# Performance work log

Hardware: AMD Instinct MI355X
Metric: run time of the kernel (lower is better)

The kernel has to match this reference:

```python
import jax, jax.numpy as jnp
import numpy as np

B, S, H = 1, 2048, 1024
NH, HD = 16, 64
WIN = 512
M_MEM, M_PER = 512, 64
SCALE = 1.0 / np.sqrt(HD)
NEG_INF = jnp.float32(-1e30)


def setup_inputs() -> dict:
    key = jax.random.key(0)
    ks = jax.random.split(key, 22)
    std = 1.0 / np.sqrt(H)
    def w(k):
        return (jax.random.normal(k, (H, H), jnp.float32) * std)
    names = ['local_wq','local_wk','local_wv','local_wo',
             'long_wq','long_wk','long_wv','long_wo',
             'mem_wq','mem_wk','mem_wv','mem_wo',
             'per_wq','per_wk','per_wv','per_wo']
    d = {n: w(ks[i]) for i, n in enumerate(names)}
    d['gate_w'] = jax.random.normal(ks[16], (4 * H, 4), jnp.float32) * 0.02
    d['gate_b'] = jnp.zeros((4,), jnp.float32)
    d['x'] = jax.random.normal(ks[17], (B, S, H), jnp.float32)
    d['memory_kv'] = jax.random.normal(ks[18], (B, M_MEM, H), jnp.float32)
    d['persona_kv'] = jax.random.normal(ks[19], (B, M_PER, H), jnp.float32)
    return d


def _split_heads(t):
    # (B, T, H) -> (B, NH, T, HD)
    b, t_, _ = t.shape
    return t.reshape(b, t_, NH, HD).transpose(0, 2, 1, 3)


def _merge_heads(t):
    b, h, t_, d = t.shape
    return t.transpose(0, 2, 1, 3).reshape(b, t_, h * d)


def _self_attn(x, wq, wk, wv, wo, mask):
    # mask: (S, S) bool, True = masked out
    q = _split_heads(x @ wq)
    k = _split_heads(x @ wk)
    v = _split_heads(x @ wv)
    scores = jnp.einsum('bhsd,bhtd->bhst', q, k) * SCALE
    scores = jnp.where(mask[None, None], NEG_INF, scores)
    a = jax.nn.softmax(scores, axis=-1)
    out = jnp.einsum('bhst,bhtd->bhsd', a, v)
    return _merge_heads(out) @ wo


def _cross_attn(x, ctx, wq, wk, wv, wo):
    q = _split_heads(x @ wq)
    k = _split_heads(ctx @ wk)
    v = _split_heads(ctx @ wv)
    scores = jnp.einsum('bhsd,bhmd->bhsm', q, k) * SCALE
    a = jax.nn.softmax(scores, axis=-1)
    out = jnp.einsum('bhsm,bhmd->bhsd', a, v)
    return _merge_heads(out) @ wo


def reference(x, memory_kv, persona_kv,
              local_wq, local_wk, local_wv, local_wo,
              long_wq, long_wk, long_wv, long_wo,
              mem_wq, mem_wk, mem_wv, mem_wo,
              per_wq, per_wk, per_wv, per_wo,
              gate_w, gate_b):
    s = x.shape[1]
    idx = jnp.arange(s)
    causal = idx[None, :] > idx[:, None]                    # future tokens masked
    local = causal | ((idx[:, None] - idx[None, :]) > WIN)  # sliding window + causal

    local_out = _self_attn(x, local_wq, local_wk, local_wv, local_wo, local)
    long_out = _self_attn(x, long_wq, long_wk, long_wv, long_wo, causal)
    mem_out = _cross_attn(x, memory_kv, mem_wq, mem_wk, mem_wv, mem_wo)
    per_out = _cross_attn(x, persona_kv, per_wq, per_wk, per_wv, per_wo)

    outs = (local_out, long_out, mem_out, per_out)
    gate_in = jnp.concatenate(outs, axis=-1)                # (B, S, 4H)
    gates = jax.nn.softmax(gate_in @ gate_w + gate_b, axis=-1)  # (B, S, 4)
    fused = sum(gates[..., i:i + 1] * o for i, o in enumerate(outs))
    return fused  # emotion_scale = 1.0, dropout off (eval)
```

## Files before the change

### kernel.cpp

```cpp
#include <hip/hip_runtime.h>

#define S 2048
#define H 1024
#define NH 16
#define HD 64
#define WIN 512
#define SCALE_Q 0.18033688f
#define SM_SHIFT 16.0f

typedef unsigned short u16;
typedef unsigned int u32;
typedef __attribute__((ext_vector_type(8))) short bfrag;
typedef __attribute__((ext_vector_type(4))) float facc;
typedef __attribute__((ext_vector_type(4))) unsigned short u16x4;

#define VMCNT(n) asm volatile("s_waitcnt vmcnt(" #n ")" ::: "memory")

constexpr size_t M1    = 1u << 20;
constexpr size_t WTO   = 0;
constexpr size_t XBO   = 8 * M1;
constexpr size_t MEMBO = 10 * M1;
constexpr size_t PERBO = MEMBO + (M1 >> 1);
constexpr size_t QO    = PERBO + (M1 >> 4);
constexpr size_t KVO   = QO + 8 * M1;
constexpr size_t K2O   = KVO + 8 * M1;
constexpr size_t V2O   = K2O + (M1 >> 1);
constexpr size_t K3O   = V2O + (M1 >> 1);
constexpr size_t V3O   = K3O + (M1 >> 4);
constexpr size_t VT1O  = V3O + (M1 >> 4);
constexpr size_t VT2O  = VT1O + 2 * M1;
constexpr size_t VT3O  = VT2O + (M1 >> 1);
constexpr size_t RECSZ = 8704;

__device__ __forceinline__ u16 f2bf(float f) {
    union { float f; unsigned u; } v; v.f = f;
    unsigned r = v.u + 0x7fffu + ((v.u >> 16) & 1u);
    return (u16)(r >> 16);
}
__device__ __forceinline__ float bf2f(u16 b) {
    union { unsigned u; float f; } v; v.u = ((unsigned)b) << 16;
    return v.f;
}
__device__ __forceinline__ void gload16(const u16* g, u16* l) {
    __builtin_amdgcn_global_load_lds(
        (const __attribute__((address_space(1))) u32*)g,
        (__attribute__((address_space(3))) u32*)l, 16, 0, 0);
}
__device__ __forceinline__ u32 cvt_pk(float a, float b) {
    u32 w;
    asm("v_cvt_pk_bf16_f32 %0, %1, %2" : "=v"(w) : "v"(a), "v"(b));
    return w;
}
__device__ __forceinline__ void blockbar() {
    __builtin_amdgcn_sched_barrier(0);
    asm volatile("" ::: "memory");
    __builtin_amdgcn_s_barrier();
    asm volatile("" ::: "memory");
    __builtin_amdgcn_sched_barrier(0);
}

__global__ __launch_bounds__(256)
void cast_all(const float* __restrict__ x, const float* __restrict__ mem,
              const float* __restrict__ per, u16* __restrict__ ws) {
    int i = blockIdx.x * 256 + threadIdx.x;
    const float* src; u16* dst;
    if (i < 262144)           { src = x;   dst = ws + XBO;   }
    else if (i < 327680)      { src = mem; dst = ws + MEMBO; i -= 262144; }
    else if (i < 335872)      { src = per; dst = ws + PERBO; i -= 327680; }
    else return;
    const float4* p = reinterpret_cast<const float4*>(src) + (size_t)i * 2;
    float4 a = p[0], b = p[1];
    u16x4 o0, o1;
    o0[0] = f2bf(a.x); o0[1] = f2bf(a.y); o0[2] = f2bf(a.z); o0[3] = f2bf(a.w);
    o1[0] = f2bf(b.x); o1[1] = f2bf(b.y); o1[2] = f2bf(b.z); o1[3] = f2bf(b.w);
    u16x4* q = reinterpret_cast<u16x4*>(dst) + (size_t)i * 2;
    q[0] = o0; q[1] = o1;
}

__global__ __launch_bounds__(256)
void transp_cast8(const float* __restrict__ w0, const float* __restrict__ w1,
                  const float* __restrict__ w2, const float* __restrict__ w3,
                  const float* __restrict__ w4, const float* __restrict__ w5,
                  const float* __restrict__ w6, const float* __restrict__ w7,
                  u16* __restrict__ wt) {
    __shared__ float t[64][65];
    const float* wp[8] = {w0, w1, w2, w3, w4, w5, w6, w7};
    const float* w = wp[blockIdx.z];
    u16* o = wt + (size_t)blockIdx.z * (1024 * 1024);
    const int kt = blockIdx.y * 64, nt = blockIdx.x * 64;
    const int r = threadIdx.x >> 4, c4 = (threadIdx.x & 15) * 4;
#pragma unroll
    for (int p = 0; p < 4; p++) {
        float4 v = *reinterpret_cast<const float4*>(
            &w[(size_t)(kt + r + p * 16) * 1024 + nt + c4]);
        t[r + p * 16][c4 + 0] = v.x; t[r + p * 16][c4 + 1] = v.y;
        t[r + p * 16][c4 + 2] = v.z; t[r + p * 16][c4 + 3] = v.w;
    }
    __syncthreads();
#pragma unroll
    for (int p = 0; p < 4; p++) {
        int nn = r + p * 16;
        u16x4 ov;
        ov[0] = f2bf(t[c4 + 0][nn]); ov[1] = f2bf(t[c4 + 1][nn]);
        ov[2] = f2bf(t[c4 + 2][nn]); ov[3] = f2bf(t[c4 + 3][nn]);
        *reinterpret_cast<u16x4*>(&o[(size_t)(nt + nn) * 1024 + kt + c4]) = ov;
    }
}

__global__ __launch_bounds__(256)
void transp_v(u16* __restrict__ ws) {
    const int z = blockIdx.z;
    const int Skv = (z < 2) ? 2048 : (z == 2 ? 512 : 64);
    const int kb = blockIdx.x;
    if (kb * 64 >= Skv) return;
    const int h = blockIdx.y;
    const u16* V = ws + (z == 0 ? KVO + 2 * M1 : z == 1 ? KVO + 6 * M1
                       : z == 2 ? V2O : V3O);
    u16* VT = ws + (z == 0 ? XBO : z == 1 ? VT1O : z == 2 ? VT2O : VT3O);
    __shared__ __align__(16) u16 t[64][72];
    {
        const int r = threadIdx.x >> 3, c8 = (threadIdx.x & 7) * 8;
#pragma unroll
        for (int p = 0; p < 2; p++) {
            int rr = r + p * 32;
            bfrag v = *reinterpret_cast<const bfrag*>(
                &V[(size_t)(kb * 64 + rr) * 1024 + h * 64 + c8]);
            *reinterpret_cast<bfrag*>(&t[rr][c8]) = v;
        }
    }
    __syncthreads();
    {
        const int d = threadIdx.x & 63;
        const int k8b = (threadIdx.x >> 6) * 8;
#pragma unroll
        for (int p = 0; p < 2; p++) {
            int k8 = k8b + p * 32;
            bfrag o;
#pragma unroll
            for (int j = 0; j < 8; j++) o[j] = (short)t[k8 + j][d];
            *reinterpret_cast<bfrag*>(
                &VT[(size_t)(h * 64 + d) * Skv + kb * 64 + k8]) = o;
        }
    }
}

__global__ __launch_bounds__(512, 2)
void gemm256(const u16* __restrict__ A, const u16* __restrict__ Bt,
             u16* __restrict__ C, long sB, long sC, int scaleMask) {
    __shared__ __align__(16) u16 sa[2][256 * 64];
    __shared__ __align__(16) u16 sb[2][256 * 64];
    Bt += (size_t)blockIdx.z * sB;
    C  += (size_t)blockIdx.z * sC;
    const float scl = ((scaleMask >> blockIdx.z) & 1) ? SCALE_Q : 1.0f;
    const int tid = threadIdx.x;
    const int wid = tid >> 6, lane = tid & 63;
    const int lhi = lane >> 4, llo = lane & 15;
    const int wm = wid >> 2, wn = wid & 3;
    const int row0 = blockIdx.y * 256, col0 = blockIdx.x * 256;

    facc acc[8][4];
#pragma unroll
    for (int i = 0; i < 8; i++)
#pragma unroll
        for (int j = 0; j < 4; j++)
#pragma unroll
            for (int k = 0; k < 4; k++) acc[i][j][k] = 0.f;

    auto stageB = [&](int kt, int h) {
        const int b = kt & 1, k0 = kt * 64;
#pragma unroll
        for (int pass = 0; pass < 2; pass++) {
            int i = pass * 512 + tid;
            int r = h * 128 + (i >> 3);
            int ck = (i & 7) ^ (r & 7);
            gload16(&Bt[(size_t)(col0 + r) * 1024 + k0 + ck * 8],
                    &sb[b][(size_t)(h * 1024 + pass * 512 + wid * 64) * 8]);
        }
    };
    auto stageAg = [&](int kt, int g) {
        const int b = kt & 1, k0 = kt * 64;
#pragma unroll
        for (int pass = 0; pass < 2; pass++) {
            int i = pass * 512 + tid;
            int i8 = i >> 3;
            int r = g * 64 + (i8 & 63) + (i8 >> 6) * 128;
            int ck = (i & 7) ^ (r & 7);
            int b8 = (pass * 512 + wid * 64) >> 3;
            int rb = g * 64 + (b8 & 63) + (b8 >> 6) * 128;
            gload16(&A[(size_t)(row0 + r) * 1024 + k0 + ck * 8],
                    &sa[b][(size_t)rb * 64]);
        }
    };

    stageB(0, 0); stageB(0, 1); stageAg(0, 0); stageAg(0, 1);
    __builtin_amdgcn_sched_barrier(0);
    VMCNT(2);
    blockbar();

    for (int j = 0; j < 16; j++) {
        const int b = j & 1;
        const u16* pa = &sa[b][0];
        const u16* pb = &sb[b][0];
        bfrag bf[4][2];
#pragma unroll
        for (int q = 0; q < 4; q++) {
            if (q == 0) {
#pragma unroll
                for (int nf = 0; nf < 4; nf++)
#pragma unroll
                    for (int ks = 0; ks < 2; ks++) {
                        int r = wn * 64 + nf * 16 + llo;
                        int p = (ks * 4 + lhi) ^ (r & 7);
                        bf[nf][ks] = *reinterpret_cast<const bfrag*>(
                            &pb[r * 64 + p * 8]);
                    }
            }
            bfrag af[2][2];
#pragma unroll
            for (int rr = 0; rr < 2; rr++)
#pragma unroll
                for (int ks = 0; ks < 2; ks++) {
                    int r = wm * 128 + (q * 2 + rr) * 16 + llo;
                    int p = (ks * 4 + lhi) ^ (r & 7);
                    af[rr][ks] = *reinterpret_cast<const bfrag*>(
                        &pa[r * 64 + p * 8]);
                }
            if (j < 15) {
                if (q == 0)      stageB(j + 1, 0);
                else if (q == 1) stageB(j + 1, 1);
                else if (q == 2) stageAg(j + 1, 0);
                else             stageAg(j + 1, 1);
            }
            blockbar();
            asm volatile("s_waitcnt lgkmcnt(0)" ::: "memory");
            __builtin_amdgcn_sched_barrier(0);
            __builtin_amdgcn_s_setprio(1);
#pragma unroll
            for (int rr = 0; rr < 2; rr++)
#pragma unroll
                for (int nf = 0; nf < 4; nf++)
#pragma unroll
                    for (int ks = 0; ks < 2; ks++)
                        acc[q * 2 + rr][nf] = __builtin_amdgcn_mfma_f32_16x16x32_bf16(
                            af[rr][ks], bf[nf][ks], acc[q * 2 + rr][nf], 0, 0, 0);
            __builtin_amdgcn_s_setprio(0);
            __builtin_amdgcn_sched_barrier(0);
            if (q == 1) { if (j < 15) { VMCNT(4); } else { VMCNT(0); } }
            else if (q == 3 && j < 15) { VMCNT(2); }
            blockbar();
        }
    }

#pragma unroll
    for (int mf = 0; mf < 8; mf++) {
#pragma unroll
        for (int r = 0; r < 4; r++) {
            int row = row0 + wm * 128 + mf * 16 + lhi * 4 + r;
#pragma unroll
            for (int nf = 0; nf < 4; nf++) {
                int col = col0 + wn * 64 + nf * 16 + llo;
                C[(size_t)row * 1024 + col] = f2bf(acc[mf][nf][r] * scl);
            }
        }
    }
}

__device__ __forceinline__ void gemm128_body(
    const u16* __restrict__ A, const u16* __restrict__ Bt, u16* __restrict__ C,
    int M, float scl, u16* sa, u16* sb, int row0, int col0) {
    const int tid = threadIdx.x;
    const int wid = tid >> 6, lane = tid & 63;
    const int lhi = lane >> 4, llo = lane & 15;
    const int wm = wid >> 1, wn = wid & 1;

    facc acc[4][4];
#pragma unroll
    for (int i = 0; i < 4; i++)
#pragma unroll
        for (int j = 0; j < 4; j++)
#pragma unroll
            for (int k = 0; k < 4; k++) acc[i][j][k] = 0.f;

    const int srow = lane >> 3, schunk = lane & 7;
    for (int kt = 0; kt < 16; kt++) {
        __syncthreads();
        const int k0 = kt * 64;
#pragma unroll
        for (int j = 0; j < 4; j++) {
            int r = wid * 32 + j * 8 + srow;
            int ck = schunk ^ (r & 7);
            int ar = row0 + r; if (ar > M - 1) ar = M - 1;
            gload16(&A[(size_t)ar * 1024 + k0 + ck * 8], &sa[(wid * 4 + j) * 512]);
            gload16(&Bt[(size_t)(col0 + r) * 1024 + k0 + ck * 8], &sb[(wid * 4 + j) * 512]);
        }
        __syncthreads();
#pragma unroll
        for (int ks = 0; ks < 2; ks++) {
            bfrag af[4], bfv[4];
#pragma unroll
            for (int mf = 0; mf < 4; mf++) {
                int r = wm * 64 + mf * 16 + llo;
                int p = (ks * 4 + lhi) ^ (r & 7);
                af[mf] = *reinterpret_cast<const bfrag*>(&sa[r * 64 + p * 8]);
            }
#pragma unroll
            for (int nf = 0; nf < 4; nf++) {
                int r = wn * 64 + nf * 16 + llo;
                int p = (ks * 4 + lhi) ^ (r & 7);
                bfv[nf] = *reinterpret_cast<const bfrag*>(&sb[r * 64 + p * 8]);
            }
            __builtin_amdgcn_s_setprio(1);
#pragma unroll
            for (int mf = 0; mf < 4; mf++)
#pragma unroll
                for (int nf = 0; nf < 4; nf++)
                    acc[mf][nf] = __builtin_amdgcn_mfma_f32_16x16x32_bf16(
                        af[mf], bfv[nf], acc[mf][nf], 0, 0, 0);
            __builtin_amdgcn_s_setprio(0);
        }
    }
#pragma unroll
    for (int mf = 0; mf < 4; mf++) {
#pragma unroll
        for (int r = 0; r < 4; r++) {
            int row = row0 + wm * 64 + mf * 16 + lhi * 4 + r;
            if (row < M) {
#pragma unroll
                for (int nf = 0; nf < 4; nf++) {
                    int col = col0 + wn * 64 + nf * 16 + llo;
                    C[(size_t)row * 1024 + col] = f2bf(acc[mf][nf][r] * scl);
                }
            }
        }
    }
}

__global__ __launch_bounds__(256)
void gemm_bf16(const u16* __restrict__ A, const u16* __restrict__ Bt,
               u16* __restrict__ C, int M, long sA, long sB, long sC,
               int scaleMask) {
    __shared__ __align__(16) u16 sa[128 * 64];
    __shared__ __align__(16) u16 sb[128 * 64];
    A  += (size_t)blockIdx.z * sA;
    Bt += (size_t)blockIdx.z * sB;
    C  += (size_t)blockIdx.z * sC;
    const float scl = ((scaleMask >> blockIdx.z) & 1) ? SCALE_Q : 1.0f;
    gemm128_body(A, Bt, C, M, scl, sa, sb, blockIdx.y * 128, blockIdx.x * 128);
}

__global__ __launch_bounds__(256)
void gemm_small(u16* __restrict__ ws) {
    const int z = blockIdx.z;
    if (z >= 2 && blockIdx.y > 0) return;
    __shared__ __align__(16) u16 sa[128 * 64];
    __shared__ __align__(16) u16 sb[128 * 64];
    const u16* A = ws + ((z < 2) ? MEMBO : PERBO);
    const int M = (z < 2) ? 512 : 64;
    const u16* Bt = ws + WTO + (size_t)z * M1;
    u16* C = ws + (z == 0 ? K2O : z == 1 ? V2O : z == 2 ? K3O : V3O);
    gemm128_body(A, Bt, C, M, 1.0f, sa, sb, blockIdx.y * 128, blockIdx.x * 128);
}

__global__ __launch_bounds__(256)
void attn_tiled(u16* __restrict__ ws) {
    __shared__ __align__(16) u16 ksm[64 * 64];
    __shared__ __align__(16) u16 vtm[64 * 64];
    __shared__ __align__(16) u16 psm[4][16][72];

    const int blk = blockIdx.x;
    int branch, h, qb, pair = 0, half = 0;
    bool partial = false;
    if (blk < 256) {
        pair = blk >> 1; half = blk & 1;
        qb = 15 - (pair >> 4); h = pair & 15;
        branch = 1; partial = true;
    } else if (blk < 384) { int t = blk - 256; branch = 1; qb = 7 - (t >> 4);  h = t & 15; }
    else if (blk < 640)   { int t = blk - 384; branch = 0; qb = 15 - (t >> 4); h = t & 15; }
    else if (blk < 896)   { int t = blk - 640; branch = 2; qb = t >> 4;        h = t & 15; }
    else                  { int t = blk - 896; branch = 3; qb = t >> 4;        h = t & 15; }

    size_t kb_, vb_; int Skv, maskMode;
    if (branch == 0)      { kb_ = KVO;          vb_ = XBO;  Skv = 2048; maskMode = 2; }
    else if (branch == 1) { kb_ = KVO + 4 * M1; vb_ = VT1O; Skv = 2048; maskMode = 1; }
    else if (branch == 2) { kb_ = K2O;          vb_ = VT2O; Skv = 512;  maskMode = 0; }
    else                  { kb_ = K3O;          vb_ = VT3O; Skv = 64;   maskMode = 0; }
    const u16* Kp  = ws + kb_;
    const u16* VTp = ws + vb_;
    u16* Qp = ws + QO + (size_t)branch * 2 * M1;

    const int tid = threadIdx.x, wid = tid >> 6, lane = tid & 63;
    const int llo = lane & 15, lhi = lane >> 4;
    const int q0 = qb * 128;
    const int qw = q0 + wid * 32;
    const int hoff = h * 64;

    int tBeg, tEnd;
    if (partial) {
        int n = qb + 1;
        tBeg = half * n; tEnd = tBeg + n;
    } else {
        tEnd = maskMode ? (qb * 2 + 2) : (Skv >> 6);
        tBeg = (maskMode == 2 && q0 >= WIN) ? ((q0 - WIN) >> 6) : 0;
    }
    int myBeg = tBeg, myEnd = tEnd;
    if (maskMode) { int e = ((qw + 31) >> 6) + 1; if (e < myEnd) myEnd = e; }
    if (maskMode == 2 && qw >= WIN) { int b = (qw - WIN) >> 6; if (b > myBeg) myBeg = b; }

    bfrag qf[2][2];
#pragma unroll
    for (int sub = 0; sub < 2; sub++)
#pragma unroll
        for (int ds = 0; ds < 2; ds++)
            qf[sub][ds] = *reinterpret_cast<const bfrag*>(
                &Qp[(size_t)(qw + sub * 16 + llo) * 1024 + hoff + ds * 32 + lhi * 8]);

    facc ot[2][4];
    float lsum[2] = {0.f, 0.f};
#pragma unroll
    for (int sub = 0; sub < 2; sub++)
#pragma unroll
        for (int db = 0; db < 4; db++)
#pragma unroll
            for (int k = 0; k < 4; k++) ot[sub][db][k] = 0.f;

    const int srow = lane >> 3, schunk = lane & 7;

    for (int kt = tBeg; kt < tEnd; kt++) {
        __syncthreads();
#pragma unroll
        for (int j = 0; j < 2; j++) {
            int r = wid * 16 + j * 8 + srow;
            int ck = schunk ^ (r & 7);
            gload16(&Kp[(size_t)(kt * 64 + r) * 1024 + hoff + ck * 8],
                    &ksm[(wid * 2 + j) * 512]);
            gload16(&VTp[(size_t)(hoff + r) * Skv + kt * 64 + ck * 8],
                    &vtm[(wid * 2 + j) * 512]);
        }
        __syncthreads();

        if (kt >= myBeg && kt < myEnd) {
            bfrag kf[4][2], vf[4][2];
#pragma unroll
            for (int nf = 0; nf < 4; nf++)
#pragma unroll
                for (int ds = 0; ds < 2; ds++) {
                    int r = nf * 16 + llo;
                    int p = (ds * 4 + lhi) ^ (r & 7);
                    kf[nf][ds] = *reinterpret_cast<const bfrag*>(
                        &ksm[r * 64 + p * 8]);
                }
#pragma unroll
            for (int db = 0; db < 4; db++)
#pragma unroll
                for (int ks = 0; ks < 2; ks++) {
                    int d = db * 16 + llo;
                    int p = (ks * 4 + lhi) ^ (d & 7);
                    vf[db][ks] = *reinterpret_cast<const bfrag*>(
                        &vtm[d * 64 + p * 8]);
                }

#pragma unroll
            for (int sub = 0; sub < 2; sub++) {
                const int qsb = qw + sub * 16;
                facc st[4];
#pragma unroll
                for (int nf = 0; nf < 4; nf++)
#pragma unroll
                    for (int k = 0; k < 4; k++) st[nf][k] = 0.f;
                __builtin_amdgcn_s_setprio(1);
#pragma unroll
                for (int nf = 0; nf < 4; nf++)
#pragma unroll
                    for (int ds = 0; ds < 2; ds++)
                        st[nf] = __builtin_amdgcn_mfma_f32_16x16x32_bf16(
                            kf[nf][ds], qf[sub][ds], st[nf], 0, 0, 0);
                __builtin_amdgcn_s_setprio(0);

                float s[16];
#pragma unroll
                for (int nf = 0; nf < 4; nf++)
#pragma unroll
                    for (int r = 0; r < 4; r++) s[nf * 4 + r] = st[nf][r];

                const bool needC = maskMode && (kt * 64 + 63 > qsb);
                const bool needW = (maskMode == 2) && (kt * 64 < qsb + 15 - WIN);
                if (needC || needW) {
                    const int qi = qsb + llo;
#pragma unroll
                    for (int nf = 0; nf < 4; nf++)
#pragma unroll
                        for (int r = 0; r < 4; r++) {
                            int key = kt * 64 + nf * 16 + lhi * 4 + r;
                            if ((needC && key > qi) || (needW && (qi - key) > WIN))
                                s[nf * 4 + r] = -1e30f;
                        }
                }
                float p[16];
#pragma unroll
                for (int i = 0; i < 16; i++)
                    p[i] = __builtin_amdgcn_exp2f(s[i] - SM_SHIFT);
#pragma unroll
                for (int i = 0; i < 16; i++) lsum[sub] += p[i];

#pragma unroll
                for (int nf = 0; nf < 4; nf++)
#pragma unroll
                    for (int rp = 0; rp < 2; rp++) {
                        u32 w = cvt_pk(p[nf * 4 + rp * 2], p[nf * 4 + rp * 2 + 1]);
                        *reinterpret_cast<u32*>(
                            &psm[wid][llo][nf * 16 + lhi * 4 + rp * 2]) = w;
                    }
                bfrag pf0 = *reinterpret_cast<const bfrag*>(&psm[wid][llo][lhi * 8]);
                bfrag pf1 = *reinterpret_cast<const bfrag*>(&psm[wid][llo][32 + lhi * 8]);
                __builtin_amdgcn_s_setprio(1);
#pragma unroll
                for (int db = 0; db < 4; db++) {
                    ot[sub][db] = __builtin_amdgcn_mfma_f32_16x16x32_bf16(
                        vf[db][0], pf0, ot[sub][db], 0, 0, 0);
                    ot[sub][db] = __builtin_amdgcn_mfma_f32_16x16x32_bf16(
                        vf[db][1], pf1, ot[sub][db], 0, 0, 0);
                }
                __builtin_amdgcn_s_setprio(0);
            }
        }
    }

    if (!partial) {
#pragma unroll
        for (int sub = 0; sub < 2; sub++) {
            float l = lsum[sub];
            l += __shfl_xor(l, 16);
            l += __shfl_xor(l, 32);
            float inv = 1.f / l;
            u16* orow = &Qp[(size_t)(qw + sub * 16 + llo) * 1024 + hoff];
#pragma unroll
            for (int db = 0; db < 4; db++) {
                u16x4 pk;
#pragma unroll
                for (int r = 0; r < 4; r++) pk[r] = f2bf(ot[sub][db][r] * inv);
                *reinterpret_cast<u16x4*>(&orow[db * 16 + lhi * 4]) = pk;
            }
        }
    } else {
        float* rec = reinterpret_cast<float*>(ws) + (size_t)(pair * 2 + half) * RECSZ;
#pragma unroll
        for (int sub = 0; sub < 2; sub++) {
            float l = lsum[sub];
            l += __shfl_xor(l, 16);
            l += __shfl_xor(l, 32);
            rec[8192 + sub * 256 + tid] = l;
#pragma unroll
            for (int db = 0; db < 4; db++)
                *reinterpret_cast<facc*>(&rec[tid * 32 + sub * 16 + db * 4]) =
                    ot[sub][db];
        }
    }
}

__global__ __launch_bounds__(256)
void combine_split(u16* __restrict__ ws) {
    const int pair = blockIdx.x;
    const int qb = 15 - (pair >> 4), h = pair & 15;
    const int tid = threadIdx.x, wid = tid >> 6, lane = tid & 63;
    const int llo = lane & 15, lhi = lane >> 4;
    const float* r0 = reinterpret_cast<const float*>(ws) + (size_t)(pair * 2) * RECSZ;
    const float* r1 = r0 + RECSZ;
    u16* Qp = ws + QO + 2 * M1;
    const int qw = qb * 128 + wid * 32;
#pragma unroll
    for (int sub = 0; sub < 2; sub++) {
        float inv = 1.f / (r0[8192 + sub * 256 + tid] + r1[8192 + sub * 256 + tid]);
        u16* orow = &Qp[(size_t)(qw + sub * 16 + llo) * 1024 + h * 64];
#pragma unroll
        for (int db = 0; db < 4; db++) {
            u16x4 pk;
#pragma unroll
            for (int r = 0; r < 4; r++) {
                float v = r0[tid * 32 + sub * 16 + db * 4 + r] +
                          r1[tid * 32 + sub * 16 + db * 4 + r];
                pk[r] = f2bf(v * inv);
            }
            *reinterpret_cast<u16x4*>(&orow[db * 16 + lhi * 4]) = pk;
        }
    }
}

__global__ __launch_bounds__(256)
void gate_fuse(const u16* __restrict__ o4, const float* __restrict__ gw,
               const float* __restrict__ gb, float* __restrict__ out) {
    const int s = blockIdx.x, tid = threadIdx.x;
    const u16* ob0 = o4 + (size_t)s * H;
    float p[4] = {0.f, 0.f, 0.f, 0.f};
    for (int b = 0; b < 4; b++) {
        const u16* obb = ob0 + b * 2 * M1;
        const float* gwb = gw + (size_t)b * H * 4;
        for (int i = tid; i < H; i += 256) {
            float xv = bf2f(obb[i]);
            float4 g4 = *reinterpret_cast<const float4*>(&gwb[(size_t)i * 4]);
            p[0] += xv * g4.x; p[1] += xv * g4.y;
            p[2] += xv * g4.z; p[3] += xv * g4.w;
        }
    }
#pragma unroll
    for (int off = 1; off < 64; off <<= 1)
#pragma unroll
        for (int j = 0; j < 4; j++) p[j] += __shfl_xor(p[j], off);
    __shared__ float red[4][4];
    if ((tid & 63) == 0) {
        int w = tid >> 6;
#pragma unroll
        for (int j = 0; j < 4; j++) red[w][j] = p[j];
    }
    __syncthreads();
    float gl[4];
#pragma unroll
    for (int j = 0; j < 4; j++)
        gl[j] = gb[j] + red[0][j] + red[1][j] + red[2][j] + red[3][j];
    float mx = fmaxf(fmaxf(gl[0], gl[1]), fmaxf(gl[2], gl[3]));
    float e[4]; float tot = 0.f;
#pragma unroll
    for (int j = 0; j < 4; j++) { e[j] = __expf(gl[j] - mx); tot += e[j]; }
    float inv = 1.f / tot;
    int d = tid * 4;
    float4 rv; rv.x = rv.y = rv.z = rv.w = 0.f;
#pragma unroll
    for (int b = 0; b < 4; b++) {
        const u16* obb = ob0 + b * 2 * M1 + d;
        float wgt = e[b] * inv;
        rv.x += wgt * bf2f(obb[0]);
        rv.y += wgt * bf2f(obb[1]);
        rv.z += wgt * bf2f(obb[2]);
        rv.w += wgt * bf2f(obb[3]);
    }
    *reinterpret_cast<float4*>(&out[(size_t)s * H + d]) = rv;
}

extern "C" void kernel_launch(void* const* d_in, const int* in_sizes, int n_in,
                              void* d_out, int out_size, void* d_ws, size_t ws_size,
                              hipStream_t stream) {
    const float* Wm[16];
    for (int i = 0; i < 16; i++) Wm[i] = (const float*)d_in[i];
    const float* gw = (const float*)d_in[16];
    const float* gb = (const float*)d_in[17];
    const float* x = (const float*)d_in[18];
    const float* mem = (const float*)d_in[19];
    const float* per = (const float*)d_in[20];
    float* out = (float*)d_out;
    u16* ws = (u16*)d_ws;

    dim3 blk(256);
    cast_all<<<dim3(1312), blk, 0, stream>>>(x, mem, per, ws);

    transp_cast8<<<dim3(16, 16, 8), blk, 0, stream>>>(
        Wm[0], Wm[4], Wm[8], Wm[12], Wm[1], Wm[2], Wm[5], Wm[6], ws + WTO);
    gemm256<<<dim3(4, 8, 8), dim3(512), 0, stream>>>(
        ws + XBO, ws + WTO, ws + QO, (long)M1, (long)(2 * M1), 0xF);

    transp_cast8<<<dim3(16, 16, 4), blk, 0, stream>>>(
        Wm[9], Wm[10], Wm[13], Wm[14], Wm[9], Wm[10], Wm[13], Wm[14], ws + WTO);
    gemm_small<<<dim3(8, 4, 4), blk, 0, stream>>>(ws);

    transp_v<<<dim3(32, 16, 4), blk, 0, stream>>>(ws);
    attn_tiled<<<dim3(1152), blk, 0, stream>>>(ws);
    combine_split<<<dim3(128), blk, 0, stream>>>(ws);

    transp_cast8<<<dim3(16, 16, 4), blk, 0, stream>>>(
        Wm[3], Wm[7], Wm[11], Wm[15], Wm[3], Wm[7], Wm[11], Wm[15], ws + WTO);
    gemm_bf16<<<dim3(8, 16, 4), blk, 0, stream>>>(
        ws + QO, ws + WTO, ws + KVO, 2048, (long)(2 * M1), (long)M1,
        (long)(2 * M1), 0);

    gate_fuse<<<dim3(S), blk, 0, stream>>>(ws + KVO, gw, gb, out);
}
```

Before: 174.4 us.

## Double-buffer K/V tiles in attention and split causal branch finer

The attention kernel now double-buffers K and V^T tiles in LDS, prefetching the next tile with async global-to-LDS loads while the current tile is computed. The causal long-range branch is split 4-way for the last query blocks and 2-way for the middle ones, and partial records are stored in bf16 inside the weight scratch area. combine_split is generalized to sum 2 or 4 partials. This aims to hide load latency and balance work across blocks, at the cost of more LDS per block, extra launches and bf16 rounding of the partial accumulators.

```diff
diff --git a/kernel.cpp b/kernel.cpp
--- a/kernel.cpp
+++ b/kernel.cpp
@@ -30,7 +30,7 @@
 constexpr size_t VT1O  = V3O + (M1 >> 4);
 constexpr size_t VT2O  = VT1O + 2 * M1;
 constexpr size_t VT3O  = VT2O + (M1 >> 1);
-constexpr size_t RECSZ = 8704;
+constexpr size_t RECSZ16 = 9216;
 
 __device__ __forceinline__ u16 f2bf(float f) {
     union { float f; unsigned u; } v; v.f = f;
@@ -363,21 +363,23 @@
 
 __global__ __launch_bounds__(256)
 void attn_tiled(u16* __restrict__ ws) {
-    __shared__ __align__(16) u16 ksm[64 * 64];
-    __shared__ __align__(16) u16 vtm[64 * 64];
+    __shared__ __align__(16) u16 ksm[2][64 * 64];
+    __shared__ __align__(16) u16 vtm[2][64 * 64];
     __shared__ __align__(16) u16 psm[4][16][72];
 
     const int blk = blockIdx.x;
-    int branch, h, qb, pair = 0, half = 0;
-    bool partial = false;
-    if (blk < 256) {
-        pair = blk >> 1; half = blk & 1;
-        qb = 15 - (pair >> 4); h = pair & 15;
-        branch = 1; partial = true;
-    } else if (blk < 384) { int t = blk - 256; branch = 1; qb = 7 - (t >> 4);  h = t & 15; }
-    else if (blk < 640)   { int t = blk - 384; branch = 0; qb = 15 - (t >> 4); h = t & 15; }
-    else if (blk < 896)   { int t = blk - 640; branch = 2; qb = t >> 4;        h = t & 15; }
-    else                  { int t = blk - 896; branch = 3; qb = t >> 4;        h = t & 15; }
+    int branch, h, qb, piece = 0, nway = 1, rid = -1;
+    if (blk < 256)        { branch = 0; qb = 15 - (blk >> 4); h = blk & 15; }
+    else if (blk < 768)   { branch = 1; int i = blk - 256; qb = 15 - (i >> 6);
+                            int t = i & 63; h = t >> 2; piece = t & 3; nway = 4;
+                            rid = h * 40 + 8 + (qb - 8) * 4 + piece; }
+    else if (blk < 896)   { branch = 1; int i = blk - 768; qb = 7 - (i >> 5);
+                            int t = i & 31; h = t >> 1; piece = t & 1; nway = 2;
+                            rid = h * 40 + (qb - 4) * 2 + piece; }
+    else if (blk < 960)   { branch = 1; int i = blk - 896; qb = 3 - (i >> 4); h = i & 15; }
+    else if (blk < 1216)  { branch = 2; int i = blk - 960; qb = i >> 4; h = i & 15; }
+    else                  { branch = 3; int i = blk - 1216; qb = i >> 4; h = i & 15; }
+    const bool partial = (rid >= 0);
 
     size_t kb_, vb_; int Skv, maskMode;
     if (branch == 0)      { kb_ = KVO;          vb_ = XBO;  Skv = 2048; maskMode = 2; }
@@ -395,12 +397,15 @@
     const int hoff = h * 64;
 
     int tBeg, tEnd;
-    if (partial) {
-        int n = qb + 1;
-        tBeg = half * n; tEnd = tBeg + n;
+    if (branch == 1) {
+        int n = qb * 2 + 2;
+        tBeg = (n * piece) / nway;
+        tEnd = (n * (piece + 1)) / nway;
+    } else if (branch == 0) {
+        tEnd = qb * 2 + 2;
+        tBeg = (q0 >= WIN) ? ((q0 - WIN) >> 6) : 0;
     } else {
-        tEnd = maskMode ? (qb * 2 + 2) : (Skv >> 6);
-        tBeg = (maskMode == 2 && q0 >= WIN) ? ((q0 - WIN) >> 6) : 0;
+        tBeg = 0; tEnd = Skv >> 6;
     }
     int myBeg = tBeg, myEnd = tEnd;
     if (maskMode) { int e = ((qw + 31) >> 6) + 1; if (e < myEnd) myEnd = e; }
@@ -424,19 +429,27 @@
             for (int k = 0; k < 4; k++) ot[sub][db][k] = 0.f;
 
     const int srow = lane >> 3, schunk = lane & 7;
-
-    for (int kt = tBeg; kt < tEnd; kt++) {
-        __syncthreads();
+    auto stage = [&](int buf, int kt) {
 #pragma unroll
         for (int j = 0; j < 2; j++) {
             int r = wid * 16 + j * 8 + srow;
             int ck = schunk ^ (r & 7);
             gload16(&Kp[(size_t)(kt * 64 + r) * 1024 + hoff + ck * 8],
-                    &ksm[(wid * 2 + j) * 512]);
+                    &ksm[buf][(wid * 2 + j) * 512]);
             gload16(&VTp[(size_t)(hoff + r) * Skv + kt * 64 + ck * 8],
-                    &vtm[(wid * 2 + j) * 512]);
-        }
-        __syncthreads();
+                    &vtm[buf][(wid * 2 + j) * 512]);
+        }
+    };
+
+    const int nt = tEnd - tBeg;
+    stage(0, tBeg);
+    if (nt > 1) stage(1, tBeg + 1);
+    __builtin_amdgcn_sched_barrier(0);
+    if (nt > 1) { VMCNT(4); } else { VMCNT(0); }
+    blockbar();
+
+    for (int kt = tBeg; kt < tEnd; kt++) {
+        const int cur = (kt - tBeg) & 1;
 
         if (kt >= myBeg && kt < myEnd) {
             bfrag kf[4][2], vf[4][2];
@@ -447,7 +460,7 @@
                     int r = nf * 16 + llo;
                     int p = (ds * 4 + lhi) ^ (r & 7);
                     kf[nf][ds] = *reinterpret_cast<const bfrag*>(
-                        &ksm[r * 64 + p * 8]);
+                        &ksm[cur][r * 64 + p * 8]);
                 }
 #pragma unroll
             for (int db = 0; db < 4; db++)
@@ -456,7 +469,7 @@
                     int d = db * 16 + llo;
                     int p = (ks * 4 + lhi) ^ (d & 7);
                     vf[db][ks] = *reinterpret_cast<const bfrag*>(
-                        &vtm[d * 64 + p * 8]);
+                        &vtm[cur][d * 64 + p * 8]);
                 }
 
 #pragma unroll
@@ -523,6 +536,13 @@
                 __builtin_amdgcn_s_setprio(0);
             }
         }
+        if (kt + 1 < tEnd) {
+            blockbar();
+            if (kt + 2 < tEnd) stage(cur, kt + 2);
+            __builtin_amdgcn_sched_barrier(0);
+            if (kt + 2 < tEnd) { VMCNT(4); } else { VMCNT(0); }
+            blockbar();
+        }
     }
 
     if (!partial) {
@@ -542,44 +562,61 @@
             }
         }
     } else {
-        float* rec = reinterpret_cast<float*>(ws) + (size_t)(pair * 2 + half) * RECSZ;
+        u16* rec = ws + WTO + (size_t)rid * RECSZ16;
+        float* lrec = reinterpret_cast<float*>(rec + 8192);
 #pragma unroll
         for (int sub = 0; sub < 2; sub++) {
             float l = lsum[sub];
             l += __shfl_xor(l, 16);
             l += __shfl_xor(l, 32);
-            rec[8192 + sub * 256 + tid] = l;
-#pragma unroll
-            for (int db = 0; db < 4; db++)
-                *reinterpret_cast<facc*>(&rec[tid * 32 + sub * 16 + db * 4]) =
-                    ot[sub][db];
+            lrec[sub * 256 + tid] = l;
+#pragma unroll
+            for (int db = 0; db < 4; db++) {
+                u16x4 pk;
+#pragma unroll
+                for (int r = 0; r < 4; r++) pk[r] = f2bf(ot[sub][db][r]);
+                *reinterpret_cast<u16x4*>(&rec[tid * 32 + sub * 16 + db * 4]) = pk;
+            }
         }
     }
 }
 
 __global__ __launch_bounds__(256)
 void combine_split(u16* __restrict__ ws) {
-    const int pair = blockIdx.x;
-    const int qb = 15 - (pair >> 4), h = pair & 15;
+    const int gi = blockIdx.x;
+    const int h = gi / 12, rem = gi % 12;
+    int qb, nway, rbase;
+    if (rem < 4) { qb = 4 + rem; nway = 2; rbase = h * 40 + rem * 2; }
+    else         { qb = 8 + (rem - 4); nway = 4; rbase = h * 40 + 8 + (rem - 4) * 4; }
     const int tid = threadIdx.x, wid = tid >> 6, lane = tid & 63;
     const int llo = lane & 15, lhi = lane >> 4;
-    const float* r0 = reinterpret_cast<const float*>(ws) + (size_t)(pair * 2) * RECSZ;
-    const float* r1 = r0 + RECSZ;
     u16* Qp = ws + QO + 2 * M1;
     const int qw = qb * 128 + wid * 32;
 #pragma unroll
     for (int sub = 0; sub < 2; sub++) {
-        float inv = 1.f / (r0[8192 + sub * 256 + tid] + r1[8192 + sub * 256 + tid]);
+        float l = 0.f;
+        float ov[16];
+#pragma unroll
+        for (int i = 0; i < 16; i++) ov[i] = 0.f;
+        for (int k = 0; k < nway; k++) {
+            const u16* rec = ws + WTO + (size_t)(rbase + k) * RECSZ16;
+            const float* lrec = reinterpret_cast<const float*>(rec + 8192);
+            l += lrec[sub * 256 + tid];
+#pragma unroll
+            for (int i = 0; i < 16; i += 4) {
+                u16x4 pk = *reinterpret_cast<const u16x4*>(
+                    &rec[tid * 32 + sub * 16 + i]);
+#pragma unroll
+                for (int r = 0; r < 4; r++) ov[i + r] += bf2f(pk[r]);
+            }
+        }
+        float inv = 1.f / l;
         u16* orow = &Qp[(size_t)(qw + sub * 16 + llo) * 1024 + h * 64];
 #pragma unroll
         for (int db = 0; db < 4; db++) {
             u16x4 pk;
 #pragma unroll
-            for (int r = 0; r < 4; r++) {
-                float v = r0[tid * 32 + sub * 16 + db * 4 + r] +
-                          r1[tid * 32 + sub * 16 + db * 4 + r];
-                pk[r] = f2bf(v * inv);
-            }
+            for (int r = 0; r < 4; r++) pk[r] = f2bf(ov[db * 4 + r] * inv);
             *reinterpret_cast<u16x4*>(&orow[db * 16 + lhi * 4]) = pk;
         }
     }
@@ -661,8 +698,8 @@
     gemm_small<<<dim3(8, 4, 4), blk, 0, stream>>>(ws);
 
     transp_v<<<dim3(32, 16, 4), blk, 0, stream>>>(ws);
-    attn_tiled<<<dim3(1152), blk, 0, stream>>>(ws);
-    combine_split<<<dim3(128), blk, 0, stream>>>(ws);
+    attn_tiled<<<dim3(1472), blk, 0, stream>>>(ws);
+    combine_split<<<dim3(192), blk, 0, stream>>>(ws);
 
     transp_cast8<<<dim3(16, 16, 4), blk, 0, stream>>>(
         Wm[3], Wm[7], Wm[11], Wm[15], Wm[3], Wm[7], Wm[11], Wm[15], ws + WTO);
```

After: 178.8 us. 1.03x slower.
